# Optimization experiments

Measured on AMD Instinct MI355X. Metric: run time of the kernel, lower is better.

Reference implementation:

```python
import jax, jax.numpy as jnp
import numpy as np

B, D, L = 32, 256, 1024        # batch, embedding_dim, compressed_len
K = 4096                       # num_embeddings (codebook size)
COMMITMENT_COST = 0.25


def setup_inputs() -> dict:
    key = jax.random.key(0)
    k1, k2 = jax.random.split(key)
    inputs = jax.random.normal(k1, (B, D, L), dtype=jnp.float32)
    embedding = jax.random.normal(k2, (K, D), dtype=jnp.float32)  # codebook
    return {"inputs": inputs, "embedding": embedding}


def reference(inputs, embedding):
    # [B, D, L] -> [B, L, D], flatten to [N, D]
    x = jnp.transpose(inputs, (0, 2, 1))
    flat = x.reshape(-1, D)  # [N, D], N = B*L

    # squared Euclidean distances to each code: [N, K]
    distances = (
        jnp.sum(flat * flat, axis=1, keepdims=True)
        + jnp.sum(embedding * embedding, axis=1)
        - 2.0 * jnp.matmul(flat, embedding.T)
    )
    encoding_indices = jnp.argmin(distances, axis=1)          # [N]
    encodings = jax.nn.one_hot(encoding_indices, K, dtype=jnp.float32)  # [N, K]

    # quantize via gather (same math as one_hot @ embedding)
    quantized = embedding[encoding_indices].reshape(x.shape)  # [B, L, D]

    # commitment loss (EMA module: only e_latent term, quantized detached)
    e_latent_loss = jnp.mean((jax.lax.stop_gradient(quantized) - x) ** 2)
    loss = COMMITMENT_COST * e_latent_loss

    # straight-through estimator
    quantized_st = x + jax.lax.stop_gradient(quantized - x)

    # perplexity from average code usage
    avg_probs = jnp.mean(encodings, axis=0)  # [K]
    perplexity = jnp.exp(-jnp.sum(avg_probs * jnp.log(avg_probs + 1e-10)))

    quantized_out = jnp.transpose(quantized_st, (0, 2, 1))  # [B, D, L]
    return (loss, quantized_out, perplexity, embedding,
            encoding_indices[:, None], encodings)
```

## Files before the change

kernel.cpp:

```cpp
#include <hip/hip_runtime.h>
#include <float.h>
#include <math.h>

typedef __attribute__((ext_vector_type(8))) short bf16x8;
typedef __attribute__((ext_vector_type(4))) float f32x4;

#define O_Q    1
#define O_PERP 8388609
#define O_EMB  8388610
#define O_IDX  9437186
#define O_ENC  9469954

#define W_CB   1048576
#define W_CNT  1052672
#define W_BS   1056768

#define MARGIN 0.01f

__device__ __forceinline__ unsigned short bf16_rne(float x) {
    unsigned u = __float_as_uint(x);
    unsigned r = u + 0x7FFFu + ((u >> 16) & 1u);
    return (unsigned short)(r >> 16);
}

__device__ __forceinline__ void gld_lds16(const void* g, void* l) {
    __builtin_amdgcn_global_load_lds(
        (const __attribute__((address_space(1))) unsigned int*)g,
        (__attribute__((address_space(3))) unsigned int*)l, 16, 0, 0);
}

__device__ __forceinline__ unsigned long long u64min(unsigned long long a, unsigned long long b){ return a < b ? a : b; }
__device__ __forceinline__ unsigned long long u64max(unsigned long long a, unsigned long long b){ return a > b ? a : b; }

__device__ __forceinline__ unsigned long long packkey(float s, int k) {
    unsigned u = __float_as_uint(s);
    u = (u & 0x80000000u) ? ~u : (u | 0x80000000u);
    return ((unsigned long long)u << 32) | (unsigned)k;
}
__device__ __forceinline__ float unpackf(unsigned long long key) {
    unsigned u = (unsigned)(key >> 32);
    u = (u & 0x80000000u) ? (u & 0x7FFFFFFFu) : ~u;
    return __uint_as_float(u);
}

__global__ __launch_bounds__(256)
void k_prep(const float* __restrict__ E, char* __restrict__ ETpk)
{
    int gid = blockIdx.x * 256 + threadIdx.x;
    int code = gid >> 5, oct = gid & 31;
    const float* ep = E + (size_t)code * 256 + oct * 8;
    float4 a = *(const float4*)ep, c4 = *(const float4*)(ep + 4);
    float v[8] = {a.x, a.y, a.z, a.w, c4.x, c4.y, c4.z, c4.w};
    unsigned hw[8], lw[8];
#pragma unroll
    for (int i = 0; i < 8; ++i) {
        unsigned short h = bf16_rne(v[i]);
        float hf = __uint_as_float((unsigned)h << 16);
        hw[i] = h; lw[i] = bf16_rne(v[i] - hf);
    }
    uint4 vh = {hw[0]|(hw[1]<<16), hw[2]|(hw[3]<<16), hw[4]|(hw[5]<<16), hw[6]|(hw[7]<<16)};
    uint4 vl = {lw[0]|(lw[1]<<16), lw[2]|(lw[3]<<16), lw[4]|(lw[5]<<16), lw[6]|(lw[7]<<16)};
    int kt = code >> 8, cf = (code >> 4) & 15, row = code & 15;
    int dtv = oct >> 2, c = oct & 3;
    size_t chunk = (size_t)(kt * 8 + dtv) * 32768;
    *(uint4*)(ETpk + chunk + (size_t)((0*16 + cf) * 64 + (c*16 + row)) * 16) = vh;
    *(uint4*)(ETpk + chunk + (size_t)((1*16 + cf) * 64 + (c*16 + row)) * 16) = vl;
}

__global__ __launch_bounds__(256)
void k_cbias(const float* __restrict__ E, float* __restrict__ cb)
{
    const int tid = threadIdx.x;
    const int k   = blockIdx.x * 16 + (tid >> 4);
    const int ch  = tid & 15;
    const float* p = E + (size_t)k * 256 + ch * 16;
    float s = 0.f;
#pragma unroll
    for (int i = 0; i < 4; ++i) {
        float4 v = *(const float4*)(p + i * 4);
        s += v.x*v.x + v.y*v.y + v.z*v.z + v.w*v.w;
    }
#pragma unroll
    for (int m = 1; m < 16; m <<= 1) s += __shfl_xor(s, m, 64);
    if (ch == 0) cb[k] = 0.5f * s;
}

__global__ __launch_bounds__(512, 1)
void k_main(const float* __restrict__ X, const char* __restrict__ ETpk,
            const float* __restrict__ cbh, const float* __restrict__ E,
            float* __restrict__ out, int* __restrict__ counts,
            float* __restrict__ bscore)
{
    extern __shared__ char lds[];

    const int tid  = threadIdx.x;
    const int lane = tid & 63;
    const int wid  = tid >> 6;
    const int wm   = wid >> 2;
    const int wn   = wid & 3;
    const int n0   = blockIdx.x * 128;
    const int b    = n0 >> 10;
    const int l0   = n0 & 1023;
    const int tokA = tid & 127;
    const int octA = tid >> 7;

    f32x4 acc[4][4];
#pragma unroll
    for (int mi = 0; mi < 4; ++mi)
#pragma unroll
        for (int nj = 0; nj < 4; ++nj) acc[mi][nj] = (f32x4){0.f,0.f,0.f,0.f};

    float s1[16], s2[16];
    unsigned ipack[16];
#pragma unroll
    for (int s = 0; s < 16; ++s) { s1[s] = FLT_MAX; s2[s] = FLT_MAX; ipack[s] = 0; }

    const size_t xbase = (size_t)b * 262144 + l0;
    float* encB = out + (size_t)O_ENC + (size_t)n0 * 4096;

    auto stageB = [&](int rnd, int bufsel) {
        const char* src = ETpk + (size_t)rnd * 32768;
        char* dst = lds + 32768 + bufsel * 32768;
#pragma unroll
        for (int i = 0; i < 4; ++i)
            gld_lds16(src + i*8192 + tid*16, dst + i*8192 + tid*16);
    };
    auto loadA = [&](int rnd, float* xa) {
        const float* src = X + xbase + (size_t)((rnd & 7) * 32 + octA * 8) * 1024 + tokA;
#pragma unroll
        for (int i = 0; i < 8; ++i) xa[i] = src[(size_t)i * 1024];
    };
    auto writeA = [&](int bufsel, const float* xa) {
        unsigned hw[8], lw[8];
#pragma unroll
        for (int i = 0; i < 8; ++i) {
            unsigned short h16 = bf16_rne(xa[i]);
            float hf = __uint_as_float((unsigned)h16 << 16);
            hw[i] = h16; lw[i] = bf16_rne(xa[i] - hf);
        }
        uint4 vh = {hw[0]|(hw[1]<<16), hw[2]|(hw[3]<<16), hw[4]|(hw[5]<<16), hw[6]|(hw[7]<<16)};
        uint4 vl = {lw[0]|(lw[1]<<16), lw[2]|(lw[3]<<16), lw[4]|(lw[5]<<16), lw[6]|(lw[7]<<16)};
        char* dstc = lds + bufsel * 16384 + (tokA >> 4) * 1024 + (octA * 16 + (tokA & 15)) * 16;
        *(uint4*)dstc = vh;
        *(uint4*)(dstc + 8192) = vl;
    };

    {
        float xa[8];
        loadA(0, xa);
        stageB(0, 0);
        stageB(1, 1);
        writeA(0, xa);
    }
    __syncthreads();

#pragma unroll 1
    for (int rd = 0; rd < 128; ++rd) {
        const int asel = rd & 1;
        const char* A  = lds + asel * 16384;
        const char* Bp = lds + 32768 + (rd % 3) * 32768;
        float xa[8];
        loadA(rd + 1 < 128 ? rd + 1 : 127, xa);
        stageB(rd + 2 < 128 ? rd + 2 : 127, (rd + 2) % 3);
        {
            float2 z2 = make_float2(0.f, 0.f);
            float* zb = encB + (size_t)rd * 4096;
#pragma unroll
            for (int i = 0; i < 4; ++i)
                *(float2*)(zb + i * 1024 + tid * 2) = z2;
        }

        {
            bf16x8 ah[4], al[4], bt[4];
#pragma unroll
            for (int mi = 0; mi < 4; ++mi)
                ah[mi] = *(const bf16x8*)(A + (wm*4 + mi)*1024 + lane*16);
#pragma unroll
            for (int nj = 0; nj < 4; ++nj)
                bt[nj] = *(const bf16x8*)(Bp + (wn*4 + nj)*1024 + lane*16);
#pragma unroll
            for (int nj = 0; nj < 4; ++nj)
#pragma unroll
                for (int mi = 0; mi < 4; ++mi)
                    acc[mi][nj] = __builtin_amdgcn_mfma_f32_16x16x32_bf16(ah[mi], bt[nj], acc[mi][nj], 0, 0, 0);
#pragma unroll
            for (int mi = 0; mi < 4; ++mi)
                al[mi] = *(const bf16x8*)(A + 8192 + (wm*4 + mi)*1024 + lane*16);
#pragma unroll
            for (int nj = 0; nj < 4; ++nj)
#pragma unroll
                for (int mi = 0; mi < 4; ++mi)
                    acc[mi][nj] = __builtin_amdgcn_mfma_f32_16x16x32_bf16(al[mi], bt[nj], acc[mi][nj], 0, 0, 0);
#pragma unroll
            for (int nj = 0; nj < 4; ++nj)
                bt[nj] = *(const bf16x8*)(Bp + 16384 + (wn*4 + nj)*1024 + lane*16);
#pragma unroll
            for (int nj = 0; nj < 4; ++nj)
#pragma unroll
                for (int mi = 0; mi < 4; ++mi) {
                    acc[mi][nj] = __builtin_amdgcn_mfma_f32_16x16x32_bf16(ah[mi], bt[nj], acc[mi][nj], 0, 0, 0);
                    acc[mi][nj] = __builtin_amdgcn_mfma_f32_16x16x32_bf16(al[mi], bt[nj], acc[mi][nj], 0, 0, 0);
                }
        }

        if ((rd & 7) == 7) {
            const int kt = rd >> 3;
            const int cb0 = kt * 256 + wn * 64 + (lane & 15);
            float cbv[4];
#pragma unroll
            for (int nj = 0; nj < 4; ++nj) cbv[nj] = cbh[cb0 + nj * 16];
#pragma unroll
            for (int mi = 0; mi < 4; ++mi)
#pragma unroll
                for (int q = 0; q < 4; ++q) {
                    const int slot = mi * 4 + q;
#pragma unroll
                    for (int nj = 0; nj < 4; ++nj) {
                        float s = cbv[nj] - acc[mi][nj][q];
                        unsigned code = (unsigned)(cb0 + nj * 16);
                        if (s < s1[slot]) {
                            s2[slot] = s1[slot];
                            ipack[slot] = ((ipack[slot] & 0xFFFFu) << 16) | code;
                            s1[slot] = s;
                        } else if (s < s2[slot]) {
                            s2[slot] = s;
                            ipack[slot] = (ipack[slot] & 0xFFFFu) | (code << 16);
                        }
                        acc[mi][nj][q] = 0.f;
                    }
                }
        }

        writeA((rd + 1) & 1, xa);
        asm volatile("s_waitcnt vmcnt(8)" ::: "memory");
        asm volatile("s_waitcnt lgkmcnt(0)" ::: "memory");
        __builtin_amdgcn_s_barrier();
    }

    __syncthreads();

    unsigned long long key1[16], key2[16];
#pragma unroll
    for (int s = 0; s < 16; ++s) {
        key1[s] = packkey(s1[s], (int)(ipack[s] & 0xFFFFu));
        key2[s] = packkey(s2[s], (int)(ipack[s] >> 16));
    }
#pragma unroll
    for (int m = 1; m < 16; m <<= 1) {
#pragma unroll
        for (int s = 0; s < 16; ++s) {
            unsigned long long o1 = __shfl_xor(key1[s], m, 64);
            unsigned long long o2 = __shfl_xor(key2[s], m, 64);
            unsigned long long lo = u64min(key1[s], o1);
            unsigned long long hi = u64min(u64max(key1[s], o1), u64min(key2[s], o2));
            key1[s] = lo; key2[s] = hi;
        }
    }

    unsigned long long* scr = (unsigned long long*)lds;
    int* ids = (int*)(lds + 16384);
    float* wp = (float*)(lds + 16384 + 512);
    if ((lane & 15) == 0) {
#pragma unroll
        for (int mi = 0; mi < 4; ++mi)
#pragma unroll
            for (int q = 0; q < 4; ++q) {
                int slot = mi * 4 + q;
                int tl = wm * 64 + mi * 16 + ((lane >> 4) << 2) + q;
                scr[(tl * 4 + wn) * 2    ] = key1[slot];
                scr[(tl * 4 + wn) * 2 + 1] = key2[slot];
            }
    }
    __syncthreads();

    if (tid < 128) {
        unsigned long long a1 = scr[tid * 8], a2 = scr[tid * 8 + 1];
#pragma unroll
        for (int w = 1; w < 4; ++w) {
            unsigned long long b1 = scr[(tid * 4 + w) * 2];
            unsigned long long b2 = scr[(tid * 4 + w) * 2 + 1];
            unsigned long long lo = u64min(a1, b1);
            unsigned long long hi = u64min(u64max(a1, b1), u64min(a2, b2));
            a1 = lo; a2 = hi;
        }
        int k = (int)(a1 & 0xFFFFFFFFull);
        float g1 = unpackf(a1), g2 = unpackf(a2);
        if (g2 - g1 <= MARGIN) {
            int ka = k, kb = (int)(a2 & 0xFFFFFFFFull);
            float d1 = 0.f, d2 = 0.f;
            for (int d = 0; d < 256; d += 2) {
                float xv0 = X[xbase + (size_t)d * 1024 + tid];
                float xv1 = X[xbase + (size_t)(d + 1) * 1024 + tid];
                float e10 = E[(size_t)ka * 256 + d], e11 = E[(size_t)ka * 256 + d + 1];
                float e20 = E[(size_t)kb * 256 + d], e21 = E[(size_t)kb * 256 + d + 1];
                float f10 = xv0 - e10, f11 = xv1 - e11;
                float f20 = xv0 - e20, f21 = xv1 - e21;
                d1 += f10 * f10 + f11 * f11;
                d2 += f20 * f20 + f21 * f21;
            }
            if (d2 < d1 || (d2 == d1 && kb < ka)) k = kb;
        }
        ids[tid] = k;
        out[(size_t)O_IDX + n0 + tid] = (float)k;
        atomicAdd(&counts[k], 1);
        out[(size_t)O_ENC + (size_t)(n0 + tid) * 4096 + k] = 1.0f;
    }
    __syncthreads();

    float dl = 0.f;
#pragma unroll 4
    for (int r = 0; r < 64; ++r) {
        int lin = r * 512 + tid;
        int d = lin >> 7, t = lin & 127;
        float q  = E[(size_t)ids[t] * 256 + d];
        float xv = X[xbase + (size_t)d * 1024 + t];
        out[(size_t)O_Q + xbase + (size_t)d * 1024 + t] = xv + (q - xv);
        float df = q - xv;
        dl += df * df;
    }
#pragma unroll
    for (int m = 1; m < 64; m <<= 1) dl += __shfl_xor(dl, m, 64);
    if (lane == 0) wp[wid] = dl;
    __syncthreads();
    if (tid == 0) {
        float s = 0.f;
#pragma unroll
        for (int w = 0; w < 8; ++w) s += wp[w];
        bscore[blockIdx.x] = s;
    }
}

__global__ __launch_bounds__(256)
void k_final(const float* __restrict__ bscore, const int* __restrict__ counts,
             float* __restrict__ out)
{
    const int tid = threadIdx.x;
    float s = bscore[tid];
    float h = 0.f;
#pragma unroll
    for (int i = 0; i < 16; ++i) {
        float p = (float)counts[tid * 16 + i] * (1.0f / 32768.f);
        h += p * logf(p + 1e-10f);
    }
#pragma unroll
    for (int m = 1; m < 64; m <<= 1) {
        s += __shfl_xor(s, m, 64);
        h += __shfl_xor(h, m, 64);
    }
    __shared__ float rs[4], rh[4];
    if ((tid & 63) == 0) { rs[tid >> 6] = s; rh[tid >> 6] = h; }
    __syncthreads();
    if (tid == 0) {
        float S = rs[0] + rs[1] + rs[2] + rs[3];
        float H = rh[0] + rh[1] + rh[2] + rh[3];
        out[0]      = 0.25f * S / 8388608.f;
        out[O_PERP] = expf(-H);
    }
}

extern "C" void kernel_launch(void* const* d_in, const int* in_sizes, int n_in,
                              void* d_out, int out_size, void* d_ws, size_t ws_size,
                              hipStream_t stream)
{
    (void)in_sizes; (void)n_in; (void)out_size; (void)ws_size;
    const float* X = (const float*)d_in[0];
    const float* E = (const float*)d_in[1];
    float* out = (float*)d_out;
    float* ws  = (float*)d_ws;
    char*  ETpk   = (char*)ws;
    float* cbh    = ws + W_CB;
    int*   counts = (int*)(ws + W_CNT);
    float* bsc    = ws + W_BS;

    hipMemsetAsync(counts, 0, 4096 * sizeof(int), stream);
    k_prep <<<512, 256, 0, stream>>>(E, ETpk);
    k_cbias<<<256, 256, 0, stream>>>(E, cbh);
    hipFuncSetAttribute((const void*)k_main, hipFuncAttributeMaxDynamicSharedMemorySize, 131072);
    k_main <<<256, 512, 131072, stream>>>(X, ETpk, cbh, E, out, counts, bsc);
    k_final<<<1, 256, 0, stream>>>(bsc, counts, out);
    hipMemcpyAsync(out + O_EMB, E, (size_t)4096 * 256 * sizeof(float),
                   hipMemcpyDeviceToDevice, stream);
}
```

Measured before the change: 418.7 us.

## Prepack inputs to split-bf16 and drop the low-by-low MFMA term

Adds a k_prepX kernel that converts X to hi/lo bf16 pairs in the MFMA-ready tile layout inside workspace. The main kernel can then stage A tiles with global_load_lds into a unified 3-slot A+B LDS ring, instead of doing strided fp32 loads and converting in registers. Separately, the lo×lo MFMA product is removed, cutting matrix work per tile from four passes to three. The prepacked path only runs when the workspace is at least 40 MB. It costs an extra pass over X plus more LDS, and slightly reduces distance precision, which leans on the existing margin-based tie refinement.

```diff
diff --git a/kernel.cpp b/kernel.cpp
--- a/kernel.cpp
+++ b/kernel.cpp
@@ -14,6 +14,7 @@
 #define W_CB   1048576
 #define W_CNT  1052672
 #define W_BS   1056768
+#define XPK_BYTE_OFF (8u << 20)
 
 #define MARGIN 0.01f
 
@@ -44,7 +45,7 @@
 }
 
 __global__ __launch_bounds__(256)
-void k_prep(const float* __restrict__ E, char* __restrict__ ETpk)
+void k_prepE(const float* __restrict__ E, char* __restrict__ ETpk)
 {
     int gid = blockIdx.x * 256 + threadIdx.x;
     int code = gid >> 5, oct = gid & 31;
@@ -68,6 +69,37 @@
 }
 
 __global__ __launch_bounds__(256)
+void k_prepX(const float* __restrict__ X, char* __restrict__ Xpk)
+{
+    int lin = blockIdx.x * 256 + threadIdx.x;
+    int oct = lin >> 15;
+    int tok = lin & 32767;
+    int nt = tok >> 7, tokA = tok & 127;
+    int bt = tok >> 10, l = tok & 1023;
+    const float* xp = X + (size_t)bt * 262144 + l;
+    char* dst0 = Xpk + (size_t)nt * 131072 + (size_t)(tokA >> 4) * 1024
+               + (size_t)((oct << 4) | (tokA & 15)) * 16;
+#pragma unroll 1
+    for (int ks = 0; ks < 8; ++ks) {
+        float v[8];
+#pragma unroll
+        for (int i = 0; i < 8; ++i)
+            v[i] = xp[(size_t)(ks * 32 + oct * 8 + i) * 1024];
+        unsigned hw[8], lw[8];
+#pragma unroll
+        for (int i = 0; i < 8; ++i) {
+            unsigned short h = bf16_rne(v[i]);
+            float hf = __uint_as_float((unsigned)h << 16);
+            hw[i] = h; lw[i] = bf16_rne(v[i] - hf);
+        }
+        uint4 vh = {hw[0]|(hw[1]<<16), hw[2]|(hw[3]<<16), hw[4]|(hw[5]<<16), hw[6]|(hw[7]<<16)};
+        uint4 vl = {lw[0]|(lw[1]<<16), lw[2]|(lw[3]<<16), lw[4]|(lw[5]<<16), lw[6]|(lw[7]<<16)};
+        *(uint4*)(dst0 + ks * 16384)        = vh;
+        *(uint4*)(dst0 + ks * 16384 + 8192) = vl;
+    }
+}
+
+__global__ __launch_bounds__(256)
 void k_cbias(const float* __restrict__ E, float* __restrict__ cb)
 {
     const int tid = threadIdx.x;
@@ -85,11 +117,12 @@
     if (ch == 0) cb[k] = 0.5f * s;
 }
 
+template<int PRE>
 __global__ __launch_bounds__(512, 1)
 void k_main(const float* __restrict__ X, const char* __restrict__ ETpk,
-            const float* __restrict__ cbh, const float* __restrict__ E,
-            float* __restrict__ out, int* __restrict__ counts,
-            float* __restrict__ bscore)
+            const char* __restrict__ Xpk, const float* __restrict__ cbh,
+            const float* __restrict__ E, float* __restrict__ out,
+            int* __restrict__ counts, float* __restrict__ bscore)
 {
     extern __shared__ char lds[];
 
@@ -116,13 +149,21 @@
     for (int s = 0; s < 16; ++s) { s1[s] = FLT_MAX; s2[s] = FLT_MAX; ipack[s] = 0; }
 
     const size_t xbase = (size_t)b * 262144 + l0;
+    const char* XpkBlk = Xpk + (size_t)blockIdx.x * 131072;
     float* encB = out + (size_t)O_ENC + (size_t)n0 * 4096;
 
-    auto stageB = [&](int rnd, int bufsel) {
+    auto stageB = [&](int rnd, int slot) {
         const char* src = ETpk + (size_t)rnd * 32768;
-        char* dst = lds + 32768 + bufsel * 32768;
+        char* dst = lds + slot * 49152 + 16384;
 #pragma unroll
         for (int i = 0; i < 4; ++i)
+            gld_lds16(src + i*8192 + tid*16, dst + i*8192 + tid*16);
+    };
+    auto stageA = [&](int rnd, int slot) {
+        const char* src = XpkBlk + (size_t)(rnd & 7) * 16384;
+        char* dst = lds + slot * 49152;
+#pragma unroll
+        for (int i = 0; i < 2; ++i)
             gld_lds16(src + i*8192 + tid*16, dst + i*8192 + tid*16);
     };
     auto loadA = [&](int rnd, float* xa) {
@@ -130,7 +171,7 @@
 #pragma unroll
         for (int i = 0; i < 8; ++i) xa[i] = src[(size_t)i * 1024];
     };
-    auto writeA = [&](int bufsel, const float* xa) {
+    auto writeA = [&](int slot, const float* xa) {
         unsigned hw[8], lw[8];
 #pragma unroll
         for (int i = 0; i < 8; ++i) {
@@ -140,28 +181,37 @@
         }
         uint4 vh = {hw[0]|(hw[1]<<16), hw[2]|(hw[3]<<16), hw[4]|(hw[5]<<16), hw[6]|(hw[7]<<16)};
         uint4 vl = {lw[0]|(lw[1]<<16), lw[2]|(lw[3]<<16), lw[4]|(lw[5]<<16), lw[6]|(lw[7]<<16)};
-        char* dstc = lds + bufsel * 16384 + (tokA >> 4) * 1024 + (octA * 16 + (tokA & 15)) * 16;
+        char* dstc = lds + slot * 49152 + (tokA >> 4) * 1024 + (octA * 16 + (tokA & 15)) * 16;
         *(uint4*)dstc = vh;
         *(uint4*)(dstc + 8192) = vl;
     };
 
-    {
-        float xa[8];
-        loadA(0, xa);
-        stageB(0, 0);
-        stageB(1, 1);
-        writeA(0, xa);
+    if (PRE) {
+        stageA(0, 0); stageB(0, 0);
+        stageA(1, 1); stageB(1, 1);
+    } else {
+        float xa0[8];
+        loadA(0, xa0);
+        stageB(0, 0); stageB(1, 1);
+        writeA(0, xa0);
     }
     __syncthreads();
 
 #pragma unroll 1
     for (int rd = 0; rd < 128; ++rd) {
-        const int asel = rd & 1;
-        const char* A  = lds + asel * 16384;
-        const char* Bp = lds + 32768 + (rd % 3) * 32768;
+        const int slot = rd % 3;
+        const char* A  = lds + slot * 49152;
+        const char* Bp = A + 16384;
+        const int r2  = (rd + 2 < 128) ? rd + 2 : 127;
+        const int sl2 = (rd + 2) % 3;
         float xa[8];
-        loadA(rd + 1 < 128 ? rd + 1 : 127, xa);
-        stageB(rd + 2 < 128 ? rd + 2 : 127, (rd + 2) % 3);
+        if (PRE) {
+            stageA(r2, sl2);
+            stageB(r2, sl2);
+        } else {
+            loadA(rd + 1 < 128 ? rd + 1 : 127, xa);
+            stageB(r2, sl2);
+        }
         {
             float2 z2 = make_float2(0.f, 0.f);
             float* zb = encB + (size_t)rd * 4096;
@@ -197,10 +247,8 @@
 #pragma unroll
             for (int nj = 0; nj < 4; ++nj)
 #pragma unroll
-                for (int mi = 0; mi < 4; ++mi) {
+                for (int mi = 0; mi < 4; ++mi)
                     acc[mi][nj] = __builtin_amdgcn_mfma_f32_16x16x32_bf16(ah[mi], bt[nj], acc[mi][nj], 0, 0, 0);
-                    acc[mi][nj] = __builtin_amdgcn_mfma_f32_16x16x32_bf16(al[mi], bt[nj], acc[mi][nj], 0, 0, 0);
-                }
         }
 
         if ((rd & 7) == 7) {
@@ -213,27 +261,31 @@
             for (int mi = 0; mi < 4; ++mi)
 #pragma unroll
                 for (int q = 0; q < 4; ++q) {
-                    const int slot = mi * 4 + q;
+                    const int slot2 = mi * 4 + q;
 #pragma unroll
                     for (int nj = 0; nj < 4; ++nj) {
                         float s = cbv[nj] - acc[mi][nj][q];
                         unsigned code = (unsigned)(cb0 + nj * 16);
-                        if (s < s1[slot]) {
-                            s2[slot] = s1[slot];
-                            ipack[slot] = ((ipack[slot] & 0xFFFFu) << 16) | code;
-                            s1[slot] = s;
-                        } else if (s < s2[slot]) {
-                            s2[slot] = s;
-                            ipack[slot] = (ipack[slot] & 0xFFFFu) | (code << 16);
+                        if (s < s1[slot2]) {
+                            s2[slot2] = s1[slot2];
+                            ipack[slot2] = ((ipack[slot2] & 0xFFFFu) << 16) | code;
+                            s1[slot2] = s;
+                        } else if (s < s2[slot2]) {
+                            s2[slot2] = s;
+                            ipack[slot2] = (ipack[slot2] & 0xFFFFu) | (code << 16);
                         }
                         acc[mi][nj][q] = 0.f;
                     }
                 }
         }
 
-        writeA((rd + 1) & 1, xa);
-        asm volatile("s_waitcnt vmcnt(8)" ::: "memory");
-        asm volatile("s_waitcnt lgkmcnt(0)" ::: "memory");
+        if (!PRE) writeA((rd + 1) % 3, xa);
+        if (PRE) {
+            asm volatile("s_waitcnt vmcnt(10)" ::: "memory");
+        } else {
+            asm volatile("s_waitcnt vmcnt(8)" ::: "memory");
+            asm volatile("s_waitcnt lgkmcnt(0)" ::: "memory");
+        }
         __builtin_amdgcn_s_barrier();
     }
 
@@ -362,21 +414,32 @@
                               void* d_out, int out_size, void* d_ws, size_t ws_size,
                               hipStream_t stream)
 {
-    (void)in_sizes; (void)n_in; (void)out_size; (void)ws_size;
+    (void)in_sizes; (void)n_in; (void)out_size;
     const float* X = (const float*)d_in[0];
     const float* E = (const float*)d_in[1];
     float* out = (float*)d_out;
     float* ws  = (float*)d_ws;
     char*  ETpk   = (char*)ws;
+    char*  Xpk    = (char*)ws + XPK_BYTE_OFF;
     float* cbh    = ws + W_CB;
     int*   counts = (int*)(ws + W_CNT);
     float* bsc    = ws + W_BS;
 
+    const bool pre = ws_size >= (size_t)40 * 1024 * 1024;
+
     hipMemsetAsync(counts, 0, 4096 * sizeof(int), stream);
-    k_prep <<<512, 256, 0, stream>>>(E, ETpk);
+    k_prepE<<<512, 256, 0, stream>>>(E, ETpk);
     k_cbias<<<256, 256, 0, stream>>>(E, cbh);
-    hipFuncSetAttribute((const void*)k_main, hipFuncAttributeMaxDynamicSharedMemorySize, 131072);
-    k_main <<<256, 512, 131072, stream>>>(X, ETpk, cbh, E, out, counts, bsc);
+    if (pre) {
+        k_prepX<<<512, 256, 0, stream>>>(X, Xpk);
+        hipFuncSetAttribute(reinterpret_cast<const void*>(&k_main<1>),
+                            hipFuncAttributeMaxDynamicSharedMemorySize, 147456);
+        k_main<1><<<256, 512, 147456, stream>>>(X, ETpk, Xpk, cbh, E, out, counts, bsc);
+    } else {
+        hipFuncSetAttribute(reinterpret_cast<const void*>(&k_main<0>),
+                            hipFuncAttributeMaxDynamicSharedMemorySize, 147456);
+        k_main<0><<<256, 512, 147456, stream>>>(X, ETpk, Xpk, cbh, E, out, counts, bsc);
+    }
     k_final<<<1, 256, 0, stream>>>(bsc, counts, out);
     hipMemcpyAsync(out + O_EMB, E, (size_t)4096 * 256 * sizeof(float),
                    hipMemcpyDeviceToDevice, stream);
```

New measurement: 459.8 us. +9.8%, slower.

## Halve token tile per block, keep full bf16-split X tile resident in LDS

Applied to the files above, without the earlier changes.

Each block now handles 64 tokens instead of 128, so the grid doubles to 512 blocks. The whole X tile for all 256 dims is converted to hi/lo bf16 once and stored in LDS, which removes the per-round X global loads and conversions from the main loop. The matmul drops the lo*lo MFMA term, issuing three bf16 products per fragment instead of four. In exchange, every codebook tile is streamed twice as many times in total, LDS use grows to 160KB, and dropping the lo*lo term slightly reduces distance precision. That loss is partly covered by the margin-based exact recheck.

```diff
diff --git a/kernel.cpp b/kernel.cpp
--- a/kernel.cpp
+++ b/kernel.cpp
@@ -44,7 +44,7 @@
 }
 
 __global__ __launch_bounds__(256)
-void k_prep(const float* __restrict__ E, char* __restrict__ ETpk)
+void k_prepE(const float* __restrict__ E, char* __restrict__ ETpk)
 {
     int gid = blockIdx.x * 256 + threadIdx.x;
     int code = gid >> 5, oct = gid & 31;
@@ -92,115 +92,99 @@
             float* __restrict__ bscore)
 {
     extern __shared__ char lds[];
+    char* Alds = lds;
+    char* Bsl  = lds + 65536;
 
     const int tid  = threadIdx.x;
     const int lane = tid & 63;
     const int wid  = tid >> 6;
     const int wm   = wid >> 2;
     const int wn   = wid & 3;
-    const int n0   = blockIdx.x * 128;
+    const int n0   = blockIdx.x * 64;
     const int b    = n0 >> 10;
     const int l0   = n0 & 1023;
-    const int tokA = tid & 127;
-    const int octA = tid >> 7;
-
-    f32x4 acc[4][4];
-#pragma unroll
-    for (int mi = 0; mi < 4; ++mi)
-#pragma unroll
-        for (int nj = 0; nj < 4; ++nj) acc[mi][nj] = (f32x4){0.f,0.f,0.f,0.f};
-
-    float s1[16], s2[16];
-    unsigned ipack[16];
-#pragma unroll
-    for (int s = 0; s < 16; ++s) { s1[s] = FLT_MAX; s2[s] = FLT_MAX; ipack[s] = 0; }
-
     const size_t xbase = (size_t)b * 262144 + l0;
     float* encB = out + (size_t)O_ENC + (size_t)n0 * 4096;
 
-    auto stageB = [&](int rnd, int bufsel) {
+    f32x4 acc[2][4];
+#pragma unroll
+    for (int mi = 0; mi < 2; ++mi)
+#pragma unroll
+        for (int nj = 0; nj < 4; ++nj) acc[mi][nj] = (f32x4){0.f,0.f,0.f,0.f};
+
+    float s1[8], s2[8];
+    unsigned ipack[8];
+#pragma unroll
+    for (int s = 0; s < 8; ++s) { s1[s] = FLT_MAX; s2[s] = FLT_MAX; ipack[s] = 0; }
+
+    auto stageB = [&](int rnd, int slot) {
         const char* src = ETpk + (size_t)rnd * 32768;
-        char* dst = lds + 32768 + bufsel * 32768;
+        char* dst = Bsl + slot * 32768;
 #pragma unroll
         for (int i = 0; i < 4; ++i)
             gld_lds16(src + i*8192 + tid*16, dst + i*8192 + tid*16);
     };
-    auto loadA = [&](int rnd, float* xa) {
-        const float* src = X + xbase + (size_t)((rnd & 7) * 32 + octA * 8) * 1024 + tokA;
-#pragma unroll
-        for (int i = 0; i < 8; ++i) xa[i] = src[(size_t)i * 1024];
-    };
-    auto writeA = [&](int bufsel, const float* xa) {
-        unsigned hw[8], lw[8];
-#pragma unroll
-        for (int i = 0; i < 8; ++i) {
-            unsigned short h16 = bf16_rne(xa[i]);
-            float hf = __uint_as_float((unsigned)h16 << 16);
-            hw[i] = h16; lw[i] = bf16_rne(xa[i] - hf);
-        }
-        uint4 vh = {hw[0]|(hw[1]<<16), hw[2]|(hw[3]<<16), hw[4]|(hw[5]<<16), hw[6]|(hw[7]<<16)};
-        uint4 vl = {lw[0]|(lw[1]<<16), lw[2]|(lw[3]<<16), lw[4]|(lw[5]<<16), lw[6]|(lw[7]<<16)};
-        char* dstc = lds + bufsel * 16384 + (tokA >> 4) * 1024 + (octA * 16 + (tokA & 15)) * 16;
-        *(uint4*)dstc = vh;
-        *(uint4*)(dstc + 8192) = vl;
-    };
-
+
+    stageB(0, 0);
+    stageB(1, 1);
     {
-        float xa[8];
-        loadA(0, xa);
-        stageB(0, 0);
-        stageB(1, 1);
-        writeA(0, xa);
+        const int t = tid & 63;
+        const int g = tid >> 6;
+#pragma unroll
+        for (int jj = 0; jj < 4; ++jj) {
+            const int j  = g + jj * 8;
+            const int ks = j >> 2, c = j & 3;
+            const float* xp = X + xbase + (size_t)(j * 8) * 1024 + t;
+            float v[8];
+#pragma unroll
+            for (int i = 0; i < 8; ++i) v[i] = xp[(size_t)i * 1024];
+            unsigned hw[8], lw[8];
+#pragma unroll
+            for (int i = 0; i < 8; ++i) {
+                unsigned short h = bf16_rne(v[i]);
+                float hf = __uint_as_float((unsigned)h << 16);
+                hw[i] = h; lw[i] = bf16_rne(v[i] - hf);
+            }
+            uint4 vh = {hw[0]|(hw[1]<<16), hw[2]|(hw[3]<<16), hw[4]|(hw[5]<<16), hw[6]|(hw[7]<<16)};
+            uint4 vl = {lw[0]|(lw[1]<<16), lw[2]|(lw[3]<<16), lw[4]|(lw[5]<<16), lw[6]|(lw[7]<<16)};
+            char* d0 = Alds + ks * 8192 + (t >> 4) * 1024 + (c * 16 + (t & 15)) * 16;
+            *(uint4*)d0          = vh;
+            *(uint4*)(d0 + 4096) = vl;
+        }
     }
     __syncthreads();
 
 #pragma unroll 1
     for (int rd = 0; rd < 128; ++rd) {
-        const int asel = rd & 1;
-        const char* A  = lds + asel * 16384;
-        const char* Bp = lds + 32768 + (rd % 3) * 32768;
-        float xa[8];
-        loadA(rd + 1 < 128 ? rd + 1 : 127, xa);
-        stageB(rd + 2 < 128 ? rd + 2 : 127, (rd + 2) % 3);
+        const char* A  = Alds + (rd & 7) * 8192;
+        const char* Bp = Bsl + (rd % 3) * 32768;
+        const int r2  = (rd + 2 < 128) ? rd + 2 : 127;
+        stageB(r2, (rd + 2) % 3);
         {
             float2 z2 = make_float2(0.f, 0.f);
-            float* zb = encB + (size_t)rd * 4096;
-#pragma unroll
-            for (int i = 0; i < 4; ++i)
-                *(float2*)(zb + i * 1024 + tid * 2) = z2;
+            float* zb = encB + (size_t)rd * 2048 + tid * 2;
+            *(float2*)zb            = z2;
+            *(float2*)(zb + 1024)   = z2;
         }
 
         {
-            bf16x8 ah[4], al[4], bt[4];
-#pragma unroll
-            for (int mi = 0; mi < 4; ++mi)
-                ah[mi] = *(const bf16x8*)(A + (wm*4 + mi)*1024 + lane*16);
-#pragma unroll
-            for (int nj = 0; nj < 4; ++nj)
-                bt[nj] = *(const bf16x8*)(Bp + (wn*4 + nj)*1024 + lane*16);
-#pragma unroll
-            for (int nj = 0; nj < 4; ++nj)
-#pragma unroll
-                for (int mi = 0; mi < 4; ++mi)
-                    acc[mi][nj] = __builtin_amdgcn_mfma_f32_16x16x32_bf16(ah[mi], bt[nj], acc[mi][nj], 0, 0, 0);
-#pragma unroll
-            for (int mi = 0; mi < 4; ++mi)
-                al[mi] = *(const bf16x8*)(A + 8192 + (wm*4 + mi)*1024 + lane*16);
-#pragma unroll
-            for (int nj = 0; nj < 4; ++nj)
-#pragma unroll
-                for (int mi = 0; mi < 4; ++mi)
-                    acc[mi][nj] = __builtin_amdgcn_mfma_f32_16x16x32_bf16(al[mi], bt[nj], acc[mi][nj], 0, 0, 0);
-#pragma unroll
-            for (int nj = 0; nj < 4; ++nj)
-                bt[nj] = *(const bf16x8*)(Bp + 16384 + (wn*4 + nj)*1024 + lane*16);
-#pragma unroll
-            for (int nj = 0; nj < 4; ++nj)
-#pragma unroll
-                for (int mi = 0; mi < 4; ++mi) {
-                    acc[mi][nj] = __builtin_amdgcn_mfma_f32_16x16x32_bf16(ah[mi], bt[nj], acc[mi][nj], 0, 0, 0);
-                    acc[mi][nj] = __builtin_amdgcn_mfma_f32_16x16x32_bf16(al[mi], bt[nj], acc[mi][nj], 0, 0, 0);
+            bf16x8 ah[2], al[2];
+#pragma unroll
+            for (int mi = 0; mi < 2; ++mi) {
+                ah[mi] = *(const bf16x8*)(A + (wm*2 + mi)*1024 + lane*16);
+                al[mi] = *(const bf16x8*)(A + 4096 + (wm*2 + mi)*1024 + lane*16);
+            }
+#pragma unroll
+            for (int nj = 0; nj < 4; ++nj) {
+                bf16x8 bh = *(const bf16x8*)(Bp + (wn*4 + nj)*1024 + lane*16);
+                bf16x8 bl = *(const bf16x8*)(Bp + 16384 + (wn*4 + nj)*1024 + lane*16);
+#pragma unroll
+                for (int mi = 0; mi < 2; ++mi) {
+                    acc[mi][nj] = __builtin_amdgcn_mfma_f32_16x16x32_bf16(ah[mi], bh, acc[mi][nj], 0, 0, 0);
+                    acc[mi][nj] = __builtin_amdgcn_mfma_f32_16x16x32_bf16(al[mi], bh, acc[mi][nj], 0, 0, 0);
+                    acc[mi][nj] = __builtin_amdgcn_mfma_f32_16x16x32_bf16(ah[mi], bl, acc[mi][nj], 0, 0, 0);
                 }
+            }
         }
 
         if ((rd & 7) == 7) {
@@ -210,7 +194,7 @@
 #pragma unroll
             for (int nj = 0; nj < 4; ++nj) cbv[nj] = cbh[cb0 + nj * 16];
 #pragma unroll
-            for (int mi = 0; mi < 4; ++mi)
+            for (int mi = 0; mi < 2; ++mi)
 #pragma unroll
                 for (int q = 0; q < 4; ++q) {
                     const int slot = mi * 4 + q;
@@ -231,24 +215,22 @@
                 }
         }
 
-        writeA((rd + 1) & 1, xa);
-        asm volatile("s_waitcnt vmcnt(8)" ::: "memory");
-        asm volatile("s_waitcnt lgkmcnt(0)" ::: "memory");
+        asm volatile("s_waitcnt vmcnt(6)" ::: "memory");
         __builtin_amdgcn_s_barrier();
     }
 
     __syncthreads();
 
-    unsigned long long key1[16], key2[16];
-#pragma unroll
-    for (int s = 0; s < 16; ++s) {
+    unsigned long long key1[8], key2[8];
+#pragma unroll
+    for (int s = 0; s < 8; ++s) {
         key1[s] = packkey(s1[s], (int)(ipack[s] & 0xFFFFu));
         key2[s] = packkey(s2[s], (int)(ipack[s] >> 16));
     }
 #pragma unroll
     for (int m = 1; m < 16; m <<= 1) {
 #pragma unroll
-        for (int s = 0; s < 16; ++s) {
+        for (int s = 0; s < 8; ++s) {
             unsigned long long o1 = __shfl_xor(key1[s], m, 64);
             unsigned long long o2 = __shfl_xor(key2[s], m, 64);
             unsigned long long lo = u64min(key1[s], o1);
@@ -258,22 +240,22 @@
     }
 
     unsigned long long* scr = (unsigned long long*)lds;
-    int* ids = (int*)(lds + 16384);
-    float* wp = (float*)(lds + 16384 + 512);
+    int* ids  = (int*)(lds + 4096);
+    float* wp = (float*)(lds + 4096 + 256);
     if ((lane & 15) == 0) {
 #pragma unroll
-        for (int mi = 0; mi < 4; ++mi)
+        for (int mi = 0; mi < 2; ++mi)
 #pragma unroll
             for (int q = 0; q < 4; ++q) {
                 int slot = mi * 4 + q;
-                int tl = wm * 64 + mi * 16 + ((lane >> 4) << 2) + q;
+                int tl = wm * 32 + mi * 16 + ((lane >> 4) << 2) + q;
                 scr[(tl * 4 + wn) * 2    ] = key1[slot];
                 scr[(tl * 4 + wn) * 2 + 1] = key2[slot];
             }
     }
     __syncthreads();
 
-    if (tid < 128) {
+    if (tid < 64) {
         unsigned long long a1 = scr[tid * 8], a2 = scr[tid * 8 + 1];
 #pragma unroll
         for (int w = 1; w < 4; ++w) {
@@ -309,9 +291,9 @@
 
     float dl = 0.f;
 #pragma unroll 4
-    for (int r = 0; r < 64; ++r) {
+    for (int r = 0; r < 32; ++r) {
         int lin = r * 512 + tid;
-        int d = lin >> 7, t = lin & 127;
+        int d = lin >> 6, t = lin & 63;
         float q  = E[(size_t)ids[t] * 256 + d];
         float xv = X[xbase + (size_t)d * 1024 + t];
         out[(size_t)O_Q + xbase + (size_t)d * 1024 + t] = xv + (q - xv);
@@ -335,7 +317,7 @@
              float* __restrict__ out)
 {
     const int tid = threadIdx.x;
-    float s = bscore[tid];
+    float s = bscore[tid] + bscore[tid + 256];
     float h = 0.f;
 #pragma unroll
     for (int i = 0; i < 16; ++i) {
@@ -373,10 +355,11 @@
     float* bsc    = ws + W_BS;
 
     hipMemsetAsync(counts, 0, 4096 * sizeof(int), stream);
-    k_prep <<<512, 256, 0, stream>>>(E, ETpk);
+    k_prepE<<<512, 256, 0, stream>>>(E, ETpk);
     k_cbias<<<256, 256, 0, stream>>>(E, cbh);
-    hipFuncSetAttribute((const void*)k_main, hipFuncAttributeMaxDynamicSharedMemorySize, 131072);
-    k_main <<<256, 512, 131072, stream>>>(X, ETpk, cbh, E, out, counts, bsc);
+    hipFuncSetAttribute(reinterpret_cast<const void*>(&k_main),
+                        hipFuncAttributeMaxDynamicSharedMemorySize, 163840);
+    k_main <<<512, 512, 163840, stream>>>(X, ETpk, cbh, E, out, counts, bsc);
     k_final<<<1, 256, 0, stream>>>(bsc, counts, out);
     hipMemcpyAsync(out + O_EMB, E, (size_t)4096 * 256 * sizeof(float),
                    hipMemcpyDeviceToDevice, stream);
```

Result: faster. 400.4 us (-4.4%).
